# Kernel tuning notes

Hardware: AMD Instinct MI355X
Metric: run time of the kernel (lower is better)

## Reference

```python
import jax, jax.numpy as jnp
import numpy as np

B = 2048      # number of graphs
N = 256       # nodes per graph
D = 128       # node_embed_dim
H = 4         # num heads (subsets)
SUB = 32      # nodes per subset
DH = 128      # head_embed_dim
EPS = 1e-5


def setup_inputs() -> dict:
    key = jax.random.key(0)
    ks = jax.random.split(key, 4)
    subsets = np.concatenate([np.arange(h * 64, h * 64 + SUB) for h in range(H)])
    return {
        "node_embeddings": jax.random.normal(ks[0], (B * N, D), jnp.float32),
        "proj1_w": jax.random.normal(ks[1], (H, 3 * D, 2 * DH), jnp.float32) / np.float32(np.sqrt(3 * D)),
        "proj1_b": jnp.zeros((H, 2 * DH), jnp.float32),
        "gamma1": jnp.ones((2 * DH,), jnp.float32),
        "beta1": jnp.zeros((2 * DH,), jnp.float32),
        "proj2_w": jax.random.normal(ks[2], (H, 2 * DH, DH), jnp.float32) / np.float32(np.sqrt(2 * DH)),
        "proj2_b": jnp.zeros((H, DH), jnp.float32),
        "gamma2": jnp.ones((DH,), jnp.float32),
        "beta2": jnp.zeros((DH,), jnp.float32),
        "all_subset_nodes": jnp.asarray(subsets, jnp.int32),          # [H*SUB]
        "head_batch": jnp.asarray(np.repeat(np.arange(H), SUB), jnp.int32),  # [H*SUB]
        "batch": jnp.asarray(np.arange(B * N) // N, jnp.int32),      # [B*N] sorted graph ids
    }


def _layernorm(x, g, b):
    m = jnp.mean(x, axis=-1, keepdims=True)
    v = jnp.mean((x - m) ** 2, axis=-1, keepdims=True)
    return (x - m) * jax.lax.rsqrt(v + EPS) * g + b


def reference(node_embeddings, proj1_w, proj1_b, gamma1, beta1,
              proj2_w, proj2_b, gamma2, beta2,
              all_subset_nodes, head_batch, batch):
    # per-graph node offsets (mirrors torch bincount/cumsum path)
    counts_per_graph = jnp.bincount(batch, length=B)
    offsets = jnp.concatenate([jnp.zeros((1,), jnp.int32),
                               jnp.cumsum(counts_per_graph)[:-1].astype(jnp.int32)])
    flat_idx = offsets[:, None] + all_subset_nodes[None, :]   # [B, S]
    gathered = node_embeddings[flat_idx]                      # [B, S, D]

    # segment reductions over heads (sum, count, max)
    seg_sum = jax.vmap(lambda e: jax.ops.segment_sum(e, head_batch, num_segments=H))(gathered)  # [B,H,D]
    seg_max = jax.vmap(lambda e: jax.ops.segment_max(e, head_batch, num_segments=H))(gathered)  # [B,H,D]
    cnt = jax.ops.segment_sum(jnp.ones(head_batch.shape, jnp.float32), head_batch, num_segments=H)
    mean = seg_sum / jnp.clip(cnt, 1.0, None)[None, :, None]

    combined = jnp.concatenate([mean, seg_max, seg_sum], axis=-1)  # [B, H, 3D]

    h1 = jnp.einsum('bhi,hij->bhj', combined, proj1_w) + proj1_b
    h1 = jax.nn.relu(_layernorm(h1, gamma1, beta1))                # dropout is identity at eval
    out = jnp.einsum('bhi,hij->bhj', h1, proj2_w) + proj2_b
    out = jax.nn.relu(_layernorm(out, gamma2, beta2))
    return out                                                     # [B, H, DH]
```

## Files before the change

### kernel.cpp

```cpp
#include <hip/hip_runtime.h>
#include <math.h>

namespace {

constexpr int Bg   = 2048;
constexpr int Nn   = 256;
constexpr int Dd   = 128;
constexpr int Hh   = 4;
constexpr int SUBn = 32;
constexpr int DHd  = 128;
constexpr int D3   = 384;
constexpr int DH2  = 256;
constexpr int Gg   = 16;
constexpr int XP   = 392;
constexpr int HP   = 264;
constexpr float EPSf = 1e-5f;

typedef __attribute__((ext_vector_type(8))) short bf16x8;
typedef __attribute__((ext_vector_type(4))) float f32x4;

__device__ __forceinline__ unsigned short bf_rne(float f) {
    union { float f; unsigned int u; } v; v.f = f;
    const unsigned int u = v.u + 0x7FFFu + ((v.u >> 16) & 1u);
    return (unsigned short)(u >> 16);
}

__global__ __launch_bounds__(256)
void prep_k(const float* __restrict__ w1, const float* __restrict__ w2,
            const int* __restrict__ batch,
            unsigned short* __restrict__ wt1, unsigned short* __restrict__ wt2,
            int* __restrict__ offs)
{
    const int bid = (int)blockIdx.x;
    const int t   = (int)threadIdx.x;

    if (bid >= 128) {
        const int i = (bid - 128) * 256 + t;
        const int v = batch[i];
        if (i == 0 || batch[i - 1] != v) offs[v] = i;
        return;
    }

    __shared__ float tile[64][65];
    const float* src; unsigned short* dst; int K, J, k0, j0;
    if (bid < 96) {
        const int hb = bid / 24, tl = bid % 24;
        k0 = (tl % 6) * 64; j0 = (tl / 6) * 64;
        K = D3; J = DH2;
        src = w1 + (size_t)hb * D3 * DH2;
        dst = wt1 + (size_t)hb * DH2 * D3;
    } else {
        const int b2 = bid - 96, hb = b2 / 8, tl = b2 % 8;
        k0 = (tl % 4) * 64; j0 = (tl / 4) * 64;
        K = DH2; J = DHd;
        src = w2 + (size_t)hb * DH2 * DHd;
        dst = wt2 + (size_t)hb * DHd * DH2;
    }

    #pragma unroll
    for (int it = 0; it < 16; ++it) {
        const int idx = it * 256 + t;
        tile[idx >> 6][idx & 63] =
            src[(size_t)(k0 + (idx >> 6)) * J + (j0 + (idx & 63))];
    }
    __syncthreads();
    #pragma unroll
    for (int it = 0; it < 16; ++it) {
        const int idx = it * 256 + t;
        const int jr = idx >> 6, kc = idx & 63;
        dst[(size_t)(j0 + jr) * K + (k0 + kc)] = bf_rne(tile[kc][jr]);
    }
}

__global__ __launch_bounds__(256, 4)
void fused_k(const float* __restrict__ emb,
             const unsigned short* __restrict__ wt1,
             const unsigned short* __restrict__ wt2,
             const int* __restrict__ subset,
             const int* __restrict__ offs,
             const float* __restrict__ b1, const float* __restrict__ g1,
             const float* __restrict__ be1,
             const float* __restrict__ b2, const float* __restrict__ g2,
             const float* __restrict__ be2,
             float* __restrict__ out)
{
    __shared__ __align__(16) unsigned short X[Gg * XP];
    __shared__ __align__(16) unsigned short H1s[Gg * HP];
    __shared__ float red[2][4][Gg];
    __shared__ int sn[SUBn];
    __shared__ int soff[Gg];

    const int t   = (int)threadIdx.x;
    const int bid = (int)blockIdx.x;
    const int xcd = bid & 7, slot = bid >> 3;
    const int head = xcd >> 1;
    const int gblk = ((xcd & 1) << 6) + slot;
    const int gbase = gblk * Gg;

    if (t < SUBn) sn[t] = subset[head * SUBn + t];
    if (t >= 64 && t < 64 + Gg) soff[t - 64] = offs[gbase + (t - 64)];
    __syncthreads();

    {
        const int g  = t >> 4;
        const int cp = t & 15;
        const float* base = emb + (size_t)soff[g] * Dd;

        float sAx = 0.f, sAy = 0.f, sAz = 0.f, sAw = 0.f;
        float sBx = 0.f, sBy = 0.f, sBz = 0.f, sBw = 0.f;
        float mAx = -INFINITY, mAy = -INFINITY, mAz = -INFINITY, mAw = -INFINITY;
        float mBx = -INFINITY, mBy = -INFINITY, mBz = -INFINITY, mBw = -INFINITY;

        #pragma unroll 4
        for (int s = 0; s < SUBn; ++s) {
            const float* rp = base + (size_t)sn[s] * Dd;
            const float4 va = *reinterpret_cast<const float4*>(rp + cp * 4);
            const float4 vb = *reinterpret_cast<const float4*>(rp + cp * 4 + 64);
            sAx += va.x; sAy += va.y; sAz += va.z; sAw += va.w;
            sBx += vb.x; sBy += vb.y; sBz += vb.z; sBw += vb.w;
            mAx = fmaxf(mAx, va.x); mAy = fmaxf(mAy, va.y);
            mAz = fmaxf(mAz, va.z); mAw = fmaxf(mAw, va.w);
            mBx = fmaxf(mBx, vb.x); mBy = fmaxf(mBy, vb.y);
            mBz = fmaxf(mBz, vb.z); mBw = fmaxf(mBw, vb.w);
        }

        unsigned short* xr = X + g * XP;
        const int dA = cp * 4, dB = cp * 4 + 64;
        *reinterpret_cast<ushort4*>(xr + dA) =
            make_ushort4(bf_rne(sAx * 0.03125f), bf_rne(sAy * 0.03125f),
                         bf_rne(sAz * 0.03125f), bf_rne(sAw * 0.03125f));
        *reinterpret_cast<ushort4*>(xr + dB) =
            make_ushort4(bf_rne(sBx * 0.03125f), bf_rne(sBy * 0.03125f),
                         bf_rne(sBz * 0.03125f), bf_rne(sBw * 0.03125f));
        *reinterpret_cast<ushort4*>(xr + Dd + dA) =
            make_ushort4(bf_rne(mAx), bf_rne(mAy), bf_rne(mAz), bf_rne(mAw));
        *reinterpret_cast<ushort4*>(xr + Dd + dB) =
            make_ushort4(bf_rne(mBx), bf_rne(mBy), bf_rne(mBz), bf_rne(mBw));
        *reinterpret_cast<ushort4*>(xr + 2 * Dd + dA) =
            make_ushort4(bf_rne(sAx), bf_rne(sAy), bf_rne(sAz), bf_rne(sAw));
        *reinterpret_cast<ushort4*>(xr + 2 * Dd + dB) =
            make_ushort4(bf_rne(sBx), bf_rne(sBy), bf_rne(sBz), bf_rne(sBw));
    }
    __syncthreads();

    const int lane = t & 63, wv = t >> 6;
    const int lrow = lane & 15, q = lane >> 4;

    bf16x8 a1[12];
    #pragma unroll
    for (int k0 = 0; k0 < 12; ++k0)
        a1[k0] = *reinterpret_cast<const bf16x8*>(X + lrow * XP + k0 * 32 + q * 8);

    f32x4 acc[4];
    #pragma unroll
    for (int jt = 0; jt < 4; ++jt) {
        const int j = wv * 64 + jt * 16 + lrow;
        const float bj = b1[head * DH2 + j];
        f32x4 c = {bj, bj, bj, bj};
        const unsigned short* wp = wt1 + ((size_t)head * DH2 + j) * D3 + q * 8;
        #pragma unroll
        for (int k0 = 0; k0 < 12; ++k0)
            c = __builtin_amdgcn_mfma_f32_16x16x32_bf16(
                    a1[k0], *reinterpret_cast<const bf16x8*>(wp + k0 * 32), c, 0, 0, 0);
        acc[jt] = c;
    }

    {
        float s1[4], s2[4];
        #pragma unroll
        for (int r = 0; r < 4; ++r) {
            float a = acc[0][r] + acc[1][r] + acc[2][r] + acc[3][r];
            float b = acc[0][r] * acc[0][r] + acc[1][r] * acc[1][r]
                    + acc[2][r] * acc[2][r] + acc[3][r] * acc[3][r];
            #pragma unroll
            for (int m = 1; m < 16; m <<= 1) {
                a += __shfl_xor(a, m, 64);
                b += __shfl_xor(b, m, 64);
            }
            s1[r] = a; s2[r] = b;
        }
        if (lrow == 0) {
            #pragma unroll
            for (int r = 0; r < 4; ++r) {
                red[0][wv][q * 4 + r] = s1[r];
                red[1][wv][q * 4 + r] = s2[r];
            }
        }
        __syncthreads();

        float t1[4] = {0.f, 0.f, 0.f, 0.f}, t2[4] = {0.f, 0.f, 0.f, 0.f};
        #pragma unroll
        for (int w = 0; w < 4; ++w) {
            const float4 r1 = *reinterpret_cast<const float4*>(&red[0][w][q * 4]);
            const float4 r2 = *reinterpret_cast<const float4*>(&red[1][w][q * 4]);
            t1[0] += r1.x; t1[1] += r1.y; t1[2] += r1.z; t1[3] += r1.w;
            t2[0] += r2.x; t2[1] += r2.y; t2[2] += r2.z; t2[3] += r2.w;
        }
        float mean[4], rstd[4];
        #pragma unroll
        for (int r = 0; r < 4; ++r) {
            mean[r] = t1[r] * (1.f / 256.f);
            const float var = t2[r] * (1.f / 256.f) - mean[r] * mean[r];
            rstd[r] = rsqrtf(var + EPSf);
        }
        #pragma unroll
        for (int jt = 0; jt < 4; ++jt) {
            const int j = wv * 64 + jt * 16 + lrow;
            const float gj = g1[j], bj = be1[j];
            #pragma unroll
            for (int r = 0; r < 4; ++r) {
                const float h = fmaxf(0.f, (acc[jt][r] - mean[r]) * rstd[r] * gj + bj);
                H1s[(q * 4 + r) * HP + j] = bf_rne(h);
            }
        }
    }
    __syncthreads();

    bf16x8 a2[8];
    #pragma unroll
    for (int k0 = 0; k0 < 8; ++k0)
        a2[k0] = *reinterpret_cast<const bf16x8*>(H1s + lrow * HP + k0 * 32 + q * 8);

    f32x4 acc2[2];
    #pragma unroll
    for (int jt = 0; jt < 2; ++jt) {
        const int j = wv * 32 + jt * 16 + lrow;
        const float bj = b2[head * DHd + j];
        f32x4 c = {bj, bj, bj, bj};
        const unsigned short* wp = wt2 + ((size_t)head * DHd + j) * DH2 + q * 8;
        #pragma unroll
        for (int k0 = 0; k0 < 8; ++k0)
            c = __builtin_amdgcn_mfma_f32_16x16x32_bf16(
                    a2[k0], *reinterpret_cast<const bf16x8*>(wp + k0 * 32), c, 0, 0, 0);
        acc2[jt] = c;
    }

    {
        float s1[4], s2[4];
        #pragma unroll
        for (int r = 0; r < 4; ++r) {
            float a = acc2[0][r] + acc2[1][r];
            float b = acc2[0][r] * acc2[0][r] + acc2[1][r] * acc2[1][r];
            #pragma unroll
            for (int m = 1; m < 16; m <<= 1) {
                a += __shfl_xor(a, m, 64);
                b += __shfl_xor(b, m, 64);
            }
            s1[r] = a; s2[r] = b;
        }
        __syncthreads();
        if (lrow == 0) {
            #pragma unroll
            for (int r = 0; r < 4; ++r) {
                red[0][wv][q * 4 + r] = s1[r];
                red[1][wv][q * 4 + r] = s2[r];
            }
        }
        __syncthreads();

        float t1[4] = {0.f, 0.f, 0.f, 0.f}, t2[4] = {0.f, 0.f, 0.f, 0.f};
        #pragma unroll
        for (int w = 0; w < 4; ++w) {
            const float4 r1 = *reinterpret_cast<const float4*>(&red[0][w][q * 4]);
            const float4 r2 = *reinterpret_cast<const float4*>(&red[1][w][q * 4]);
            t1[0] += r1.x; t1[1] += r1.y; t1[2] += r1.z; t1[3] += r1.w;
            t2[0] += r2.x; t2[1] += r2.y; t2[2] += r2.z; t2[3] += r2.w;
        }
        #pragma unroll
        for (int r = 0; r < 4; ++r) {
            const float mean = t1[r] * (1.f / 128.f);
            const float var  = t2[r] * (1.f / 128.f) - mean * mean;
            const float rstd = rsqrtf(var + EPSf);
            #pragma unroll
            for (int jt = 0; jt < 2; ++jt) {
                const int j = wv * 32 + jt * 16 + lrow;
                const float o = fmaxf(0.f,
                    (acc2[jt][r] - mean) * rstd * g2[j] + be2[j]);
                out[(size_t)(gbase + q * 4 + r) * (Hh * DHd) + head * DHd + j] = o;
            }
        }
    }
}

}

extern "C" void kernel_launch(void* const* d_in, const int* in_sizes, int n_in,
                              void* d_out, int out_size, void* d_ws, size_t ws_size,
                              hipStream_t stream) {
    const float* emb  = (const float*)d_in[0];
    const float* w1   = (const float*)d_in[1];
    const float* b1   = (const float*)d_in[2];
    const float* g1   = (const float*)d_in[3];
    const float* be1  = (const float*)d_in[4];
    const float* w2   = (const float*)d_in[5];
    const float* b2   = (const float*)d_in[6];
    const float* g2   = (const float*)d_in[7];
    const float* be2  = (const float*)d_in[8];
    const int* subset = (const int*)d_in[9];
    const int* batch  = (const int*)d_in[11];
    float* out = (float*)d_out;

    int* offs = (int*)d_ws;
    unsigned short* wt1 = (unsigned short*)((char*)d_ws + 16384);
    unsigned short* wt2 = wt1 + (size_t)Hh * DH2 * D3;

    prep_k <<<dim3(128 + Bg * Nn / 256), dim3(256), 0, stream>>>(w1, w2, batch,
                                                                 wt1, wt2, offs);
    fused_k<<<dim3(Hh * (Bg / Gg)), dim3(256), 0, stream>>>(emb, wt1, wt2,
                                                            subset, offs,
                                                            b1, g1, be1,
                                                            b2, g2, be2, out);
}
```

Before: 46.05 us.

## Fuse prep and main kernels into one persistent launch with atomic-counter barriers

Merges the weight transpose/bf16 conversion and graph-offset computation into the main kernel, using global atomic counters and spin-waits so that all 256 blocks finish the offsets and 128 blocks finish the weight tiles before the dependent phases. The block size doubles to 512 threads, with 32 graphs per block, and each wave now computes two row tiles that share one weight fragment. This removes a kernel launch and halves the weight reads per graph. In exchange it needs a memset launch and relies on all 256 blocks being co-resident, or the spin-waits deadlock. Holding fewer A fragments in registers may also change occupancy.

```diff
diff --git a/kernel.cpp b/kernel.cpp
--- a/kernel.cpp
+++ b/kernel.cpp
@@ -11,9 +11,10 @@
 constexpr int DHd  = 128;
 constexpr int D3   = 384;
 constexpr int DH2  = 256;
-constexpr int Gg   = 16;
+constexpr int Gg   = 32;
 constexpr int XP   = 392;
 constexpr int HP   = 264;
+constexpr int NBLK = 256;
 constexpr float EPSf = 1e-5f;
 
 typedef __attribute__((ext_vector_type(8))) short bf16x8;
@@ -25,77 +26,85 @@
     return (unsigned short)(u >> 16);
 }
 
-__global__ __launch_bounds__(256)
-void prep_k(const float* __restrict__ w1, const float* __restrict__ w2,
-            const int* __restrict__ batch,
-            unsigned short* __restrict__ wt1, unsigned short* __restrict__ wt2,
-            int* __restrict__ offs)
+__global__ __launch_bounds__(512, 2)
+void fused_all(const float* __restrict__ emb,
+               const float* __restrict__ w1, const float* __restrict__ w2,
+               const float* __restrict__ b1, const float* __restrict__ g1,
+               const float* __restrict__ be1,
+               const float* __restrict__ b2, const float* __restrict__ g2,
+               const float* __restrict__ be2,
+               const int* __restrict__ subset,
+               const int* __restrict__ batch,
+               unsigned short* __restrict__ wt1,
+               unsigned short* __restrict__ wt2,
+               int* __restrict__ offs,
+               int* __restrict__ ctr,
+               float* __restrict__ out)
 {
-    const int bid = (int)blockIdx.x;
-    const int t   = (int)threadIdx.x;
-
-    if (bid >= 128) {
-        const int i = (bid - 128) * 256 + t;
-        const int v = batch[i];
-        if (i == 0 || batch[i - 1] != v) offs[v] = i;
-        return;
-    }
-
-    __shared__ float tile[64][65];
-    const float* src; unsigned short* dst; int K, J, k0, j0;
-    if (bid < 96) {
-        const int hb = bid / 24, tl = bid % 24;
-        k0 = (tl % 6) * 64; j0 = (tl / 6) * 64;
-        K = D3; J = DH2;
-        src = w1 + (size_t)hb * D3 * DH2;
-        dst = wt1 + (size_t)hb * DH2 * D3;
-    } else {
-        const int b2 = bid - 96, hb = b2 / 8, tl = b2 % 8;
-        k0 = (tl % 4) * 64; j0 = (tl / 4) * 64;
-        K = DH2; J = DHd;
-        src = w2 + (size_t)hb * DH2 * DHd;
-        dst = wt2 + (size_t)hb * DHd * DH2;
-    }
-
-    #pragma unroll
-    for (int it = 0; it < 16; ++it) {
-        const int idx = it * 256 + t;
-        tile[idx >> 6][idx & 63] =
-            src[(size_t)(k0 + (idx >> 6)) * J + (j0 + (idx & 63))];
-    }
-    __syncthreads();
-    #pragma unroll
-    for (int it = 0; it < 16; ++it) {
-        const int idx = it * 256 + t;
-        const int jr = idx >> 6, kc = idx & 63;
-        dst[(size_t)(j0 + jr) * K + (k0 + kc)] = bf_rne(tile[kc][jr]);
-    }
-}
-
-__global__ __launch_bounds__(256, 4)
-void fused_k(const float* __restrict__ emb,
-             const unsigned short* __restrict__ wt1,
-             const unsigned short* __restrict__ wt2,
-             const int* __restrict__ subset,
-             const int* __restrict__ offs,
-             const float* __restrict__ b1, const float* __restrict__ g1,
-             const float* __restrict__ be1,
-             const float* __restrict__ b2, const float* __restrict__ g2,
-             const float* __restrict__ be2,
-             float* __restrict__ out)
-{
+    __shared__ __align__(16) float tileT[64][65];
     __shared__ __align__(16) unsigned short X[Gg * XP];
     __shared__ __align__(16) unsigned short H1s[Gg * HP];
-    __shared__ float red[2][4][Gg];
+    __shared__ float red[2][8][Gg];
     __shared__ int sn[SUBn];
     __shared__ int soff[Gg];
 
     const int t   = (int)threadIdx.x;
     const int bid = (int)blockIdx.x;
-    const int xcd = bid & 7, slot = bid >> 3;
+    const int xcd = bid & 7;
     const int head = xcd >> 1;
-    const int gblk = ((xcd & 1) << 6) + slot;
+    const int gblk = ((xcd & 1) << 5) + (bid >> 3);
     const int gbase = gblk * Gg;
+
+    {
+        const int i = bid * 2048 + t * 4;
+        const int4 v = *reinterpret_cast<const int4*>(batch + i);
+        const int prev = (i == 0) ? -1 : batch[i - 1];
+        if (v.x != prev) offs[v.x] = i;
+        if (v.y != v.x)  offs[v.y] = i + 1;
+        if (v.z != v.y)  offs[v.z] = i + 2;
+        if (v.w != v.z)  offs[v.w] = i + 3;
+    }
+    __syncthreads();
+    if (t == 0)
+        __hip_atomic_fetch_add(&ctr[0], 1, __ATOMIC_RELEASE, __HIP_MEMORY_SCOPE_AGENT);
+
+    if (bid < 128) {
+        const float* src; unsigned short* dst; int K, J, k0, j0;
+        if (bid < 96) {
+            const int hb = bid / 24, tl = bid % 24;
+            k0 = (tl % 6) * 64; j0 = (tl / 6) * 64;
+            K = D3; J = DH2;
+            src = w1 + (size_t)hb * D3 * DH2;
+            dst = wt1 + (size_t)hb * DH2 * D3;
+        } else {
+            const int b2i = bid - 96, hb = b2i / 8, tl = b2i % 8;
+            k0 = (tl % 4) * 64; j0 = (tl / 4) * 64;
+            K = DH2; J = DHd;
+            src = w2 + (size_t)hb * DH2 * DHd;
+            dst = wt2 + (size_t)hb * DHd * DH2;
+        }
+        #pragma unroll
+        for (int it = 0; it < 8; ++it) {
+            const int idx = it * 512 + t;
+            tileT[idx >> 6][idx & 63] =
+                src[(size_t)(k0 + (idx >> 6)) * J + (j0 + (idx & 63))];
+        }
+        __syncthreads();
+        #pragma unroll
+        for (int it = 0; it < 8; ++it) {
+            const int idx = it * 512 + t;
+            const int jr = idx >> 6, kc = idx & 63;
+            dst[(size_t)(j0 + jr) * K + (k0 + kc)] = bf_rne(tileT[kc][jr]);
+        }
+        __syncthreads();
+        if (t == 0)
+            __hip_atomic_fetch_add(&ctr[1], 1, __ATOMIC_RELEASE, __HIP_MEMORY_SCOPE_AGENT);
+    }
+
+    if (t == 0)
+        while (__hip_atomic_load(&ctr[0], __ATOMIC_ACQUIRE, __HIP_MEMORY_SCOPE_AGENT) < NBLK)
+            __builtin_amdgcn_s_sleep(2);
+    __syncthreads();
 
     if (t < SUBn) sn[t] = subset[head * SUBn + t];
     if (t >= 64 && t < 64 + Gg) soff[t - 64] = offs[gbase + (t - 64)];
@@ -143,140 +152,148 @@
     }
     __syncthreads();
 
+    if (t == 0)
+        while (__hip_atomic_load(&ctr[1], __ATOMIC_ACQUIRE, __HIP_MEMORY_SCOPE_AGENT) < 128)
+            __builtin_amdgcn_s_sleep(2);
+    __syncthreads();
+
     const int lane = t & 63, wv = t >> 6;
     const int lrow = lane & 15, q = lane >> 4;
 
-    bf16x8 a1[12];
-    #pragma unroll
-    for (int k0 = 0; k0 < 12; ++k0)
-        a1[k0] = *reinterpret_cast<const bf16x8*>(X + lrow * XP + k0 * 32 + q * 8);
-
-    f32x4 acc[4];
-    #pragma unroll
-    for (int jt = 0; jt < 4; ++jt) {
-        const int j = wv * 64 + jt * 16 + lrow;
-        const float bj = b1[head * DH2 + j];
-        f32x4 c = {bj, bj, bj, bj};
-        const unsigned short* wp = wt1 + ((size_t)head * DH2 + j) * D3 + q * 8;
-        #pragma unroll
-        for (int k0 = 0; k0 < 12; ++k0)
-            c = __builtin_amdgcn_mfma_f32_16x16x32_bf16(
-                    a1[k0], *reinterpret_cast<const bf16x8*>(wp + k0 * 32), c, 0, 0, 0);
-        acc[jt] = c;
-    }
-
-    {
-        float s1[4], s2[4];
-        #pragma unroll
-        for (int r = 0; r < 4; ++r) {
-            float a = acc[0][r] + acc[1][r] + acc[2][r] + acc[3][r];
-            float b = acc[0][r] * acc[0][r] + acc[1][r] * acc[1][r]
-                    + acc[2][r] * acc[2][r] + acc[3][r] * acc[3][r];
-            #pragma unroll
-            for (int m = 1; m < 16; m <<= 1) {
-                a += __shfl_xor(a, m, 64);
-                b += __shfl_xor(b, m, 64);
-            }
-            s1[r] = a; s2[r] = b;
-        }
-        if (lrow == 0) {
-            #pragma unroll
-            for (int r = 0; r < 4; ++r) {
-                red[0][wv][q * 4 + r] = s1[r];
-                red[1][wv][q * 4 + r] = s2[r];
-            }
-        }
-        __syncthreads();
-
-        float t1[4] = {0.f, 0.f, 0.f, 0.f}, t2[4] = {0.f, 0.f, 0.f, 0.f};
-        #pragma unroll
-        for (int w = 0; w < 4; ++w) {
-            const float4 r1 = *reinterpret_cast<const float4*>(&red[0][w][q * 4]);
-            const float4 r2 = *reinterpret_cast<const float4*>(&red[1][w][q * 4]);
-            t1[0] += r1.x; t1[1] += r1.y; t1[2] += r1.z; t1[3] += r1.w;
-            t2[0] += r2.x; t2[1] += r2.y; t2[2] += r2.z; t2[3] += r2.w;
-        }
-        float mean[4], rstd[4];
-        #pragma unroll
-        for (int r = 0; r < 4; ++r) {
-            mean[r] = t1[r] * (1.f / 256.f);
-            const float var = t2[r] * (1.f / 256.f) - mean[r] * mean[r];
-            rstd[r] = rsqrtf(var + EPSf);
-        }
-        #pragma unroll
-        for (int jt = 0; jt < 4; ++jt) {
-            const int j = wv * 64 + jt * 16 + lrow;
-            const float gj = g1[j], bj = be1[j];
-            #pragma unroll
-            for (int r = 0; r < 4; ++r) {
-                const float h = fmaxf(0.f, (acc[jt][r] - mean[r]) * rstd[r] * gj + bj);
-                H1s[(q * 4 + r) * HP + j] = bf_rne(h);
-            }
-        }
-    }
-    __syncthreads();
-
-    bf16x8 a2[8];
-    #pragma unroll
-    for (int k0 = 0; k0 < 8; ++k0)
-        a2[k0] = *reinterpret_cast<const bf16x8*>(H1s + lrow * HP + k0 * 32 + q * 8);
-
-    f32x4 acc2[2];
+    f32x4 acc0[2], acc1[2];
     #pragma unroll
     for (int jt = 0; jt < 2; ++jt) {
         const int j = wv * 32 + jt * 16 + lrow;
-        const float bj = b2[head * DHd + j];
-        f32x4 c = {bj, bj, bj, bj};
-        const unsigned short* wp = wt2 + ((size_t)head * DHd + j) * DH2 + q * 8;
-        #pragma unroll
-        for (int k0 = 0; k0 < 8; ++k0)
-            c = __builtin_amdgcn_mfma_f32_16x16x32_bf16(
-                    a2[k0], *reinterpret_cast<const bf16x8*>(wp + k0 * 32), c, 0, 0, 0);
-        acc2[jt] = c;
-    }
-
-    {
-        float s1[4], s2[4];
+        const float bj = b1[head * DH2 + j];
+        acc0[jt] = (f32x4){bj, bj, bj, bj};
+        acc1[jt] = (f32x4){bj, bj, bj, bj};
+    }
+    #pragma unroll
+    for (int jt = 0; jt < 2; ++jt) {
+        const int j = wv * 32 + jt * 16 + lrow;
+        const unsigned short* wp = wt1 + ((size_t)head * DH2 + j) * D3 + q * 8;
+        #pragma unroll
+        for (int k0 = 0; k0 < 12; ++k0) {
+            const bf16x8 w = *reinterpret_cast<const bf16x8*>(wp + k0 * 32);
+            const bf16x8 a0 = *reinterpret_cast<const bf16x8*>(X + lrow * XP + k0 * 32 + q * 8);
+            const bf16x8 a1 = *reinterpret_cast<const bf16x8*>(X + (16 + lrow) * XP + k0 * 32 + q * 8);
+            acc0[jt] = __builtin_amdgcn_mfma_f32_16x16x32_bf16(a0, w, acc0[jt], 0, 0, 0);
+            acc1[jt] = __builtin_amdgcn_mfma_f32_16x16x32_bf16(a1, w, acc1[jt], 0, 0, 0);
+        }
+    }
+
+    {
         #pragma unroll
         for (int r = 0; r < 4; ++r) {
-            float a = acc2[0][r] + acc2[1][r];
-            float b = acc2[0][r] * acc2[0][r] + acc2[1][r] * acc2[1][r];
+            float a0 = acc0[0][r] + acc0[1][r];
+            float b0 = acc0[0][r] * acc0[0][r] + acc0[1][r] * acc0[1][r];
+            float a1 = acc1[0][r] + acc1[1][r];
+            float b1s = acc1[0][r] * acc1[0][r] + acc1[1][r] * acc1[1][r];
             #pragma unroll
             for (int m = 1; m < 16; m <<= 1) {
-                a += __shfl_xor(a, m, 64);
-                b += __shfl_xor(b, m, 64);
-            }
-            s1[r] = a; s2[r] = b;
+                a0 += __shfl_xor(a0, m, 64);  b0  += __shfl_xor(b0, m, 64);
+                a1 += __shfl_xor(a1, m, 64);  b1s += __shfl_xor(b1s, m, 64);
+            }
+            if (lrow == 0) {
+                red[0][wv][q * 4 + r]      = a0;
+                red[1][wv][q * 4 + r]      = b0;
+                red[0][wv][16 + q * 4 + r] = a1;
+                red[1][wv][16 + q * 4 + r] = b1s;
+            }
         }
         __syncthreads();
-        if (lrow == 0) {
+
+        float mean0[4], rstd0[4], mean1[4], rstd1[4];
+        #pragma unroll
+        for (int tl = 0; tl < 2; ++tl) {
+            float t1[4] = {0.f, 0.f, 0.f, 0.f}, t2[4] = {0.f, 0.f, 0.f, 0.f};
+            #pragma unroll
+            for (int w = 0; w < 8; ++w) {
+                const float4 r1 = *reinterpret_cast<const float4*>(&red[0][w][tl * 16 + q * 4]);
+                const float4 r2 = *reinterpret_cast<const float4*>(&red[1][w][tl * 16 + q * 4]);
+                t1[0] += r1.x; t1[1] += r1.y; t1[2] += r1.z; t1[3] += r1.w;
+                t2[0] += r2.x; t2[1] += r2.y; t2[2] += r2.z; t2[3] += r2.w;
+            }
             #pragma unroll
             for (int r = 0; r < 4; ++r) {
-                red[0][wv][q * 4 + r] = s1[r];
-                red[1][wv][q * 4 + r] = s2[r];
+                const float mn = t1[r] * (1.f / 256.f);
+                const float var = t2[r] * (1.f / 256.f) - mn * mn;
+                const float rs = rsqrtf(var + EPSf);
+                if (tl == 0) { mean0[r] = mn; rstd0[r] = rs; }
+                else         { mean1[r] = mn; rstd1[r] = rs; }
+            }
+        }
+
+        #pragma unroll
+        for (int jt = 0; jt < 2; ++jt) {
+            const int j = wv * 32 + jt * 16 + lrow;
+            const float gj = g1[j], bj = be1[j];
+            #pragma unroll
+            for (int r = 0; r < 4; ++r) {
+                const float h0 = fmaxf(0.f, (acc0[jt][r] - mean0[r]) * rstd0[r] * gj + bj);
+                const float h1 = fmaxf(0.f, (acc1[jt][r] - mean1[r]) * rstd1[r] * gj + bj);
+                H1s[(q * 4 + r) * HP + j]        = bf_rne(h0);
+                H1s[(16 + q * 4 + r) * HP + j]   = bf_rne(h1);
+            }
+        }
+    }
+    __syncthreads();
+
+    const int j2 = wv * 16 + lrow;
+    f32x4 c20, c21;
+    {
+        const float bj = b2[head * DHd + j2];
+        c20 = (f32x4){bj, bj, bj, bj};
+        c21 = (f32x4){bj, bj, bj, bj};
+        const unsigned short* wp = wt2 + ((size_t)head * DHd + j2) * DH2 + q * 8;
+        #pragma unroll
+        for (int k0 = 0; k0 < 8; ++k0) {
+            const bf16x8 w = *reinterpret_cast<const bf16x8*>(wp + k0 * 32);
+            const bf16x8 h0 = *reinterpret_cast<const bf16x8*>(H1s + lrow * HP + k0 * 32 + q * 8);
+            const bf16x8 h1 = *reinterpret_cast<const bf16x8*>(H1s + (16 + lrow) * HP + k0 * 32 + q * 8);
+            c20 = __builtin_amdgcn_mfma_f32_16x16x32_bf16(h0, w, c20, 0, 0, 0);
+            c21 = __builtin_amdgcn_mfma_f32_16x16x32_bf16(h1, w, c21, 0, 0, 0);
+        }
+    }
+
+    {
+        #pragma unroll
+        for (int r = 0; r < 4; ++r) {
+            float a0 = c20[r], b0 = c20[r] * c20[r];
+            float a1 = c21[r], b1s = c21[r] * c21[r];
+            #pragma unroll
+            for (int m = 1; m < 16; m <<= 1) {
+                a0 += __shfl_xor(a0, m, 64);  b0  += __shfl_xor(b0, m, 64);
+                a1 += __shfl_xor(a1, m, 64);  b1s += __shfl_xor(b1s, m, 64);
+            }
+            if (lrow == 0) {
+                red[0][wv][q * 4 + r]      = a0;
+                red[1][wv][q * 4 + r]      = b0;
+                red[0][wv][16 + q * 4 + r] = a1;
+                red[1][wv][16 + q * 4 + r] = b1s;
             }
         }
         __syncthreads();
 
-        float t1[4] = {0.f, 0.f, 0.f, 0.f}, t2[4] = {0.f, 0.f, 0.f, 0.f};
-        #pragma unroll
-        for (int w = 0; w < 4; ++w) {
-            const float4 r1 = *reinterpret_cast<const float4*>(&red[0][w][q * 4]);
-            const float4 r2 = *reinterpret_cast<const float4*>(&red[1][w][q * 4]);
-            t1[0] += r1.x; t1[1] += r1.y; t1[2] += r1.z; t1[3] += r1.w;
-            t2[0] += r2.x; t2[1] += r2.y; t2[2] += r2.z; t2[3] += r2.w;
-        }
-        #pragma unroll
-        for (int r = 0; r < 4; ++r) {
-            const float mean = t1[r] * (1.f / 128.f);
-            const float var  = t2[r] * (1.f / 128.f) - mean * mean;
-            const float rstd = rsqrtf(var + EPSf);
-            #pragma unroll
-            for (int jt = 0; jt < 2; ++jt) {
-                const int j = wv * 32 + jt * 16 + lrow;
-                const float o = fmaxf(0.f,
-                    (acc2[jt][r] - mean) * rstd * g2[j] + be2[j]);
-                out[(size_t)(gbase + q * 4 + r) * (Hh * DHd) + head * DHd + j] = o;
+        const float gj = g2[j2], bj = be2[j2];
+        #pragma unroll
+        for (int tl = 0; tl < 2; ++tl) {
+            float t1[4] = {0.f, 0.f, 0.f, 0.f}, t2[4] = {0.f, 0.f, 0.f, 0.f};
+            #pragma unroll
+            for (int w = 0; w < 8; ++w) {
+                const float4 r1 = *reinterpret_cast<const float4*>(&red[0][w][tl * 16 + q * 4]);
+                const float4 r2 = *reinterpret_cast<const float4*>(&red[1][w][tl * 16 + q * 4]);
+                t1[0] += r1.x; t1[1] += r1.y; t1[2] += r1.z; t1[3] += r1.w;
+                t2[0] += r2.x; t2[1] += r2.y; t2[2] += r2.z; t2[3] += r2.w;
+            }
+            #pragma unroll
+            for (int r = 0; r < 4; ++r) {
+                const float mn = t1[r] * (1.f / 128.f);
+                const float var = t2[r] * (1.f / 128.f) - mn * mn;
+                const float rs = rsqrtf(var + EPSf);
+                const float v = (tl == 0) ? c20[r] : c21[r];
+                const float o = fmaxf(0.f, (v - mn) * rs * gj + bj);
+                out[(size_t)(gbase + tl * 16 + q * 4 + r) * (Hh * DHd) + head * DHd + j2] = o;
             }
         }
     }
@@ -300,14 +317,15 @@
     const int* batch  = (const int*)d_in[11];
     float* out = (float*)d_out;
 
-    int* offs = (int*)d_ws;
+    int* ctr  = (int*)d_ws;
+    int* offs = (int*)((char*)d_ws + 256);
     unsigned short* wt1 = (unsigned short*)((char*)d_ws + 16384);
     unsigned short* wt2 = wt1 + (size_t)Hh * DH2 * D3;
 
-    prep_k <<<dim3(128 + Bg * Nn / 256), dim3(256), 0, stream>>>(w1, w2, batch,
-                                                                 wt1, wt2, offs);
-    fused_k<<<dim3(Hh * (Bg / Gg)), dim3(256), 0, stream>>>(emb, wt1, wt2,
-                                                            subset, offs,
-                                                            b1, g1, be1,
-                                                            b2, g2, be2, out);
+    hipMemsetAsync(ctr, 0, 8, stream);
+    fused_all<<<dim3(NBLK), dim3(512), 0, stream>>>(emb, w1, w2,
+                                                    b1, g1, be1,
+                                                    b2, g2, be2,
+                                                    subset, batch,
+                                                    wt1, wt2, offs, ctr, out);
 }
```

Result: slower. 61.62 us (+33.8%).
